# Kernel optimization log

Measured on AMD Instinct MI355X. Metric: run time of the kernel, lower is better.

Reference implementation:

```python
import jax, jax.numpy as jnp
import numpy as np

B, S, D = 4, 1024, 768
H = 12
DK = D // H            # 64
NUM_EMB = 10
MAX_DIST = 100000.0 * 2 ** 0.5
POS_SCALE = 100000.0   # tile positions live in [0, 100000]


def setup_inputs() -> dict:
    key = jax.random.key(0)
    ks = jax.random.split(key, 12)
    query = jax.random.normal(ks[0], (B, S, D), dtype=jnp.float32)
    key_t = jax.random.normal(ks[1], (B, S, D), dtype=jnp.float32)
    value = jax.random.normal(ks[2], (B, S, D), dtype=jnp.float32)
    tile_positions = jax.random.uniform(ks[3], (B, S, 2), dtype=jnp.float32) * POS_SCALE
    # Linear weights, torch layout [out, in]; xavier_uniform init, zero bias
    lim = float(np.sqrt(6.0 / (D + D)))
    Wq = jax.random.uniform(ks[4], (D, D), minval=-lim, maxval=lim, dtype=jnp.float32)
    Wk = jax.random.uniform(ks[5], (D, D), minval=-lim, maxval=lim, dtype=jnp.float32)
    Wv = jax.random.uniform(ks[6], (D, D), minval=-lim, maxval=lim, dtype=jnp.float32)
    bq = jnp.zeros((D,), jnp.float32)
    bk = jnp.zeros((D,), jnp.float32)
    bv = jnp.zeros((D,), jnp.float32)
    emb_k = jax.random.normal(ks[7], (NUM_EMB, DK), dtype=jnp.float32)  # nn.Embedding default N(0,1)
    return {"query": query, "key": key_t, "value": value,
            "tile_positions": tile_positions,
            "Wq": Wq, "bq": bq, "Wk": Wk, "bk": bk, "Wv": Wv, "bv": bv,
            "emb_k": emb_k}


def reference(query, key, value, tile_positions, Wq, bq, Wk, bk, Wv, bv, emb_k):
    b, s, _ = query.shape
    # projections -> [B, H, S, DK]
    q = (query @ Wq.T + bq).reshape(b, s, H, DK).transpose(0, 2, 1, 3)
    k = (key   @ Wk.T + bk).reshape(b, s, H, DK).transpose(0, 2, 1, 3)
    v = (value @ Wv.T + bv).reshape(b, s, H, DK).transpose(0, 2, 1, 3)
    # pairwise distances, normalized, discretized to embedding indices
    pos = jax.lax.stop_gradient(tile_positions)
    diff = pos[:, :, None, :] - pos[:, None, :, :]          # [B,S,S,2]
    dist = jnp.sqrt(jnp.sum(diff * diff, axis=-1)) / MAX_DIST  # [B,S,S]
    idx = jnp.clip(jnp.round(dist * (NUM_EMB - 1)), 0, NUM_EMB - 1).astype(jnp.int32)
    rk = emb_k[idx]                                          # [B,S,S,DK]
    # logits: QK^T plus distance-aware key bias
    attn_logits = jnp.einsum('bhqd,bhkd->bhqk', q, k)
    attn_logits = attn_logits + jnp.einsum('bhqd,bqkd->bhqk', q, rk)
    attn_logits = attn_logits / (DK ** 0.5)
    attention = jax.nn.softmax(attn_logits, axis=-1)
    out = jnp.einsum('bhqk,bhkd->bhqd', attention, v)       # [B,H,S,DK]
    out = out.transpose(0, 2, 1, 3).reshape(b, s, -1)       # [B,S,D]
    return out
```

## Files before the change

kernel.cpp:

```cpp
#include <hip/hip_runtime.h>
#include <hip/hip_bf16.h>

#define Bsz 4
#define Ssz 1024
#define Dsz 768
#define Hn 12
#define DKsz 64
#define NUMEMB 10

#define IDX_OFF 64
#define K_OFF   4194368
#define V_OFF   10485824
#define WBF_OFF 16777280
#define XBF_OFF 20316224
#define WS_TIER_B 20316224ULL
#define WS_TIER_A 39190592ULL

#define NXz 3145728
#define NWz 589824

typedef __attribute__((ext_vector_type(8))) short short8;
typedef __attribute__((ext_vector_type(8))) float float8;
typedef __attribute__((ext_vector_type(4))) float f32x4;
typedef __attribute__((ext_vector_type(4))) unsigned int u32x4;
typedef __attribute__((ext_vector_type(2))) unsigned int u32x2;
typedef __attribute__((ext_vector_type(4))) short s16x4;

__device__ __forceinline__ float bfbits2f(short u) {
    union { unsigned int i; float f; } v;
    v.i = ((unsigned int)(unsigned short)u) << 16;
    return v.f;
}
__device__ __forceinline__ unsigned short f2bf_bits(float f) {
    __hip_bfloat16 h = __float2bfloat16(f);
    return *reinterpret_cast<unsigned short*>(&h);
}

template<bool BF16>
__device__ __forceinline__ float loadf(const void* base, size_t idx) {
    if constexpr (BF16) return __bfloat162float(((const __hip_bfloat16*)base)[idx]);
    else return ((const float*)base)[idx];
}
template<bool BF16>
__device__ __forceinline__ short8 load8bf(const void* base, size_t idx) {
    if constexpr (BF16) {
        return *(const short8*)((const short*)base + idx);
    } else {
        float8 f = *(const float8*)((const float*)base + idx);
        short8 r;
#pragma unroll
        for (int i = 0; i < 8; i++) r[i] = (short)f2bf_bits(f[i]);
        return r;
    }
}
template<bool BF16>
__device__ __forceinline__ float8 load8f(const void* base, size_t idx) {
    if constexpr (BF16) {
        short8 s = *(const short8*)((const short*)base + idx);
        float8 f;
#pragma unroll
        for (int i = 0; i < 8; i++) f[i] = bfbits2f(s[i]);
        return f;
    } else {
        return *(const float8*)((const float*)base + idx);
    }
}

__global__ __launch_bounds__(64) void detect_kernel(
    const unsigned int* __restrict__ q, const unsigned int* __restrict__ p,
    const unsigned int* __restrict__ w, const unsigned int* __restrict__ e,
    int* __restrict__ flags)
{
    const int which = blockIdx.x;
    const unsigned int* ptr = (which == 0) ? q : ((which == 1) ? p : ((which == 2) ? w : e));
    const int n = (which == 3) ? 320 : ((which == 1) ? 4096 : 1024);
    int cnt = 0;
    for (int i = threadIdx.x; i < n; i += 64) {
        const unsigned int ex = (ptr[i] >> 7) & 0xFF;
        cnt += (ex >= 110 && ex <= 145) ? 1 : 0;
    }
#pragma unroll
    for (int off = 1; off < 64; off <<= 1) cnt += __shfl_xor(cnt, off, 64);
    if (threadIdx.x == 0) flags[which] = (2 * cnt > n) ? 1 : 0;
}

__global__ __launch_bounds__(256) void conv_kernel(
    const void* __restrict__ X0, const void* __restrict__ X1, const void* __restrict__ X2,
    const void* __restrict__ W0, const void* __restrict__ W1, const void* __restrict__ W2,
    const int* __restrict__ flags, short* __restrict__ Xbf, short* __restrict__ Wbf,
    int doX)
{
    const long t = (long)blockIdx.x * 256 + threadIdx.x;
    const bool xb = flags[0] != 0, wb = flags[2] != 0;
    if (doX) {
        const long i8 = t * 8;
        if (i8 < (long)3 * NXz) {
            const int z = (int)(i8 / NXz);
            const long off = i8 - (long)z * NXz;
            const void* X = (z == 0) ? X0 : ((z == 1) ? X1 : X2);
            short8 v = xb ? load8bf<true>(X, off) : load8bf<false>(X, off);
            *(short8*)(Xbf + i8) = v;
        } else {
            const long j = i8 - (long)3 * NXz;
            const int z = (int)(j / NWz);
            const long off = j - (long)z * NWz;
            const void* W = (z == 0) ? W0 : ((z == 1) ? W1 : W2);
            short8 v = wb ? load8bf<true>(W, off) : load8bf<false>(W, off);
            *(short8*)(Wbf + j) = v;
        }
    } else {
        const long j = t * 8;
        const int z = (int)(j / NWz);
        const long off = j - (long)z * NWz;
        const void* W = (z == 0) ? W0 : ((z == 1) ? W1 : W2);
        short8 v = wb ? load8bf<true>(W, off) : load8bf<false>(W, off);
        *(short8*)(Wbf + j) = v;
    }
}

template<bool PB>
__device__ __forceinline__ void idx_body(
    const void* pos, unsigned char* __restrict__ idxb)
{
    const int kt = blockIdx.x, qt = blockIdx.y, b = blockIdx.z;
    const int t = threadIdx.x;
    const int r = t >> 2, cc = t & 3;
    const int q = qt * 64 + r;
    const float qx = loadf<PB>(pos, ((size_t)b * Ssz + q) * 2);
    const float qy = loadf<PB>(pos, ((size_t)b * Ssz + q) * 2 + 1);
    const float MAXD = 141421.35623730951f;
    const int k0 = kt * 64 + cc * 16;
    unsigned int w[4];
#pragma unroll
    for (int g = 0; g < 4; g++) {
        unsigned int acc = 0;
#pragma unroll
        for (int u = 0; u < 4; u++) {
            const int k = k0 + g * 4 + u;
            const float kx = loadf<PB>(pos, ((size_t)b * Ssz + k) * 2);
            const float ky = loadf<PB>(pos, ((size_t)b * Ssz + k) * 2 + 1);
            const float dx = __fsub_rn(qx, kx);
            const float dy = __fsub_rn(qy, ky);
            const float ss = __fadd_rn(__fmul_rn(dx, dx), __fmul_rn(dy, dy));
            const float dist = __fdiv_rn(sqrtf(ss), MAXD);
            const float d9 = __fmul_rn(dist, 9.0f);
            int idx = (int)rintf(d9);
            idx = idx < 0 ? 0 : (idx > NUMEMB - 1 ? NUMEMB - 1 : idx);
            acc |= ((unsigned int)idx) << (8 * u);
        }
        w[g] = acc;
    }
    u32x4 v; v[0] = w[0]; v[1] = w[1]; v[2] = w[2]; v[3] = w[3];
    *(u32x4*)(idxb + ((size_t)(b * Ssz + q)) * Ssz + k0) = v;
}

__global__ __launch_bounds__(256) void idx_kernel(
    const void* pos, const int* __restrict__ flags, unsigned char* __restrict__ idxb)
{
    if (flags[1] != 0) idx_body<true >(pos, idxb);
    else               idx_body<false>(pos, idxb);
}

template<bool XB, bool WB>
__device__ __forceinline__ void proj_body(
    const void* X, const void* W, const void* bias, bool biasbf, void* Y, bool ybf,
    int zmode, int bx, int by, short* As, short* Bs)
{
    const int tid  = threadIdx.x;
    const int wave = tid >> 6;
    const int lane = tid & 63;
    const int l15  = lane & 15;
    const int quad = lane >> 4;
    const int wm = wave & 1;
    const int wn = wave >> 1;
    const int m0 = bx * 64;
    const int n0 = by * 128;

    f32x4 acc[2][4];
#pragma unroll
    for (int i = 0; i < 2; i++)
#pragma unroll
        for (int j = 0; j < 4; j++) acc[i][j] = (f32x4)0.0f;

    const int r0 = tid >> 3;
    const int cc = tid & 7;

    short8 pa0 = load8bf<XB>(X, (size_t)(m0 + r0)      * Dsz + cc * 8);
    short8 pa1 = load8bf<XB>(X, (size_t)(m0 + 32 + r0) * Dsz + cc * 8);
    short8 pb0 = load8bf<WB>(W, (size_t)(n0 + r0)      * Dsz + cc * 8);
    short8 pb1 = load8bf<WB>(W, (size_t)(n0 + 32 + r0) * Dsz + cc * 8);
    short8 pb2 = load8bf<WB>(W, (size_t)(n0 + 64 + r0) * Dsz + cc * 8);
    short8 pb3 = load8bf<WB>(W, (size_t)(n0 + 96 + r0) * Dsz + cc * 8);

    for (int kk = 0; kk < Dsz; kk += 64) {
        __syncthreads();
        *(short8*)&As[(r0)      * 72 + cc * 8] = pa0;
        *(short8*)&As[(32 + r0) * 72 + cc * 8] = pa1;
        *(short8*)&Bs[(r0)      * 72 + cc * 8] = pb0;
        *(short8*)&Bs[(32 + r0) * 72 + cc * 8] = pb1;
        *(short8*)&Bs[(64 + r0) * 72 + cc * 8] = pb2;
        *(short8*)&Bs[(96 + r0) * 72 + cc * 8] = pb3;
        __syncthreads();

        if (kk + 64 < Dsz) {
            const int k2 = kk + 64 + cc * 8;
            pa0 = load8bf<XB>(X, (size_t)(m0 + r0)      * Dsz + k2);
            pa1 = load8bf<XB>(X, (size_t)(m0 + 32 + r0) * Dsz + k2);
            pb0 = load8bf<WB>(W, (size_t)(n0 + r0)      * Dsz + k2);
            pb1 = load8bf<WB>(W, (size_t)(n0 + 32 + r0) * Dsz + k2);
            pb2 = load8bf<WB>(W, (size_t)(n0 + 64 + r0) * Dsz + k2);
            pb3 = load8bf<WB>(W, (size_t)(n0 + 96 + r0) * Dsz + k2);
        }

#pragma unroll
        for (int st = 0; st < 2; st++) {
            short8 af[2], bf[4];
#pragma unroll
            for (int i = 0; i < 2; i++)
                af[i] = *(const short8*)&As[(wm * 32 + i * 16 + l15) * 72 + st * 32 + quad * 8];
#pragma unroll
            for (int j = 0; j < 4; j++)
                bf[j] = *(const short8*)&Bs[(wn * 64 + j * 16 + l15) * 72 + st * 32 + quad * 8];
#pragma unroll
            for (int i = 0; i < 2; i++)
#pragma unroll
                for (int j = 0; j < 4; j++)
                    acc[i][j] = __builtin_amdgcn_mfma_f32_16x16x32_bf16(af[i], bf[j], acc[i][j], 0, 0, 0);
        }
    }

#pragma unroll
    for (int j = 0; j < 4; j++) {
        const int n = n0 + wn * 64 + j * 16 + l15;
        const float bv_ = biasbf ? loadf<true>(bias, n) : loadf<false>(bias, n);
        const int hh = n >> 6, dk = n & 63;
#pragma unroll
        for (int i = 0; i < 2; i++) {
            const int ms = m0 + wm * 32 + i * 16 + quad * 4;
            const int bb = ms >> 10;
            const int s0 = ms & 1023;
            if (zmode == 2) {
                s16x4 pkv;
#pragma unroll
                for (int r = 0; r < 4; r++) pkv[r] = (short)f2bf_bits(acc[i][j][r] + bv_);
                *(s16x4*)((short*)Y + (((size_t)bb * Hn + hh) * DKsz + dk) * Ssz + s0) = pkv;
            } else if (zmode == 1) {
#pragma unroll
                for (int r = 0; r < 4; r++)
                    ((__hip_bfloat16*)Y)[(((size_t)bb * Hn + hh) * Ssz + (s0 + r)) * DKsz + dk] =
                        __float2bfloat16(acc[i][j][r] + bv_);
            } else {
#pragma unroll
                for (int r = 0; r < 4; r++) {
                    const float val = acc[i][j][r] + bv_;
                    const size_t oi = (size_t)(ms + r) * Dsz + n;
                    if (ybf) ((__hip_bfloat16*)Y)[oi] = __float2bfloat16(val);
                    else     ((float*)Y)[oi] = val;
                }
            }
        }
    }
}

__global__ __launch_bounds__(256) void proj_kernel(
    const void* X0, const void* X1, const void* X2,
    const void* Wq, const void* bq, const void* Wk, const void* bk,
    const void* Wv, const void* bv,
    void* Qw, void* Kw, void* Vw, const int* __restrict__ flags,
    int fx, int fw)
{
    __shared__ __align__(16) short As[64 * 72];
    __shared__ __align__(16) short Bs[128 * 72];
    const int z = blockIdx.z;
    const void* X = (z == 0) ? X0 : ((z == 1) ? X1 : X2);
    const void* W = (z == 0) ? Wq : ((z == 1) ? Wk : Wv);
    const void* B = (z == 0) ? bq : ((z == 1) ? bk : bv);
    void* Y = (z == 0) ? Qw : ((z == 1) ? Kw : Vw);
    const bool xb = fx || flags[0] != 0;
    const bool wb = fw || flags[2] != 0;
    const bool biasbf = flags[2] != 0;
    const bool ybf = (flags[0] != 0) || (z != 0);
    if (xb) { if (wb) proj_body<true , true >(X, W, B, biasbf, Y, ybf, z, blockIdx.x, blockIdx.y, As, Bs);
              else    proj_body<true , false>(X, W, B, biasbf, Y, ybf, z, blockIdx.x, blockIdx.y, As, Bs); }
    else    { if (wb) proj_body<false, true >(X, W, B, biasbf, Y, ybf, z, blockIdx.x, blockIdx.y, As, Bs);
              else    proj_body<false, false>(X, W, B, biasbf, Y, ybf, z, blockIdx.x, blockIdx.y, As, Bs); }
}

template<bool QB, bool EB>
__device__ __forceinline__ void attn_body(
    const void* Qw, const short* __restrict__ Ks, const short* __restrict__ Vs,
    const unsigned char* __restrict__ idxb, const void* __restrict__ emb, void* out,
    unsigned short* Klds, unsigned short* Vtlds, float* qe)
{
    const int qt = blockIdx.x, h = blockIdx.y, b = blockIdx.z;
    const int tid  = threadIdx.x;
    const int wave = tid >> 6;
    const int lane = tid & 63;
    const int l15  = lane & 15;
    const int quad = lane >> 4;

    const float CSC = 0.18033688011112042f;

    for (int p = tid; p < 64 * NUMEMB; p += 256) {
        const int row = p / NUMEMB, e = p - row * NUMEMB;
        const size_t qoff = ((size_t)b * Ssz + qt * 64 + row) * Dsz + h * DKsz;
        float s = 0.f;
#pragma unroll
        for (int c = 0; c < 8; c++) {
            short8 qv = load8bf<QB>(Qw, qoff + c * 8);
            float8 ef = load8f<EB>(emb, (size_t)e * DKsz + c * 8);
#pragma unroll
            for (int i = 0; i < 8; i++) s += bfbits2f(qv[i]) * ef[i];
        }
        qe[p] = s * CSC;
    }

    short8 qfrag[2];
    {
        const size_t qbase = ((size_t)b * Ssz + qt * 64 + wave * 16 + l15) * Dsz + h * DKsz;
        qfrag[0] = load8bf<QB>(Qw, qbase + quad * 8);
        qfrag[1] = load8bf<QB>(Qw, qbase + 32 + quad * 8);
    }

    float m_run = -1e30f, l_run = 0.f;
    f32x4 oacc[4];
#pragma unroll
    for (int j = 0; j < 4; j++) oacc[j] = (f32x4)0.0f;

    const int r0 = tid >> 3, cc = tid & 7;
    const int ksl = (cc + 4 * (r0 & 1) - r0) & 7;
    const int kwoff = r0 * 72 + ksl * 8;
    const int vwoff = r0 * 72 + cc * 8;

    int koff[4][2];
#pragma unroll
    for (int jb = 0; jb < 4; jb++) {
        const int krow = (jb & 2) * 16 + (l15 >> 2) * 8 + (jb & 1) * 4 + (l15 & 3);
        const int base = quad + 4 * (l15 & 1) - (l15 & 3) + 8;
#pragma unroll
        for (int st = 0; st < 2; st++)
            koff[jb][st] = krow * 72 + ((base + 4 * (st ^ (jb & 1))) & 7) * 8;
    }

    const short* kp = Ks + ((size_t)(b * Hn + h) * Ssz) * DKsz + tid * 8;
    const short* vp = Vs + ((size_t)(b * Hn + h) * DKsz + r0) * Ssz + cc * 8;
    const unsigned char* ip = idxb + ((size_t)b * Ssz + qt * 64 + wave * 16 + l15) * Ssz + quad * 8;
    const int qrow10 = (wave * 16 + l15) * NUMEMB;

    short8 pk0 = *(const short8*)(kp);
    short8 pk1 = *(const short8*)(kp + 2048);
    short8 pv0 = *(const short8*)(vp);
    short8 pv1 = *(const short8*)(vp + 32 * Ssz);
    u32x2 idA = *(const u32x2*)(ip);
    u32x2 idB = *(const u32x2*)(ip + 32);

    *(short8*)&Klds[kwoff]            = pk0;
    *(short8*)&Klds[32 * 72 + kwoff]  = pk1;
    *(short8*)&Vtlds[vwoff]           = pv0;
    *(short8*)&Vtlds[32 * 72 + vwoff] = pv1;
    __syncthreads();

    for (int it = 0; it < 16; ++it) {
        const int cur = (it & 1) ? (64 * 72) : 0;
        const int nxt = (it & 1) ? 0 : (64 * 72);
        const unsigned int jd[4] = { idA[0], idA[1], idB[0], idB[1] };

        if (it + 1 < 16) {
            kp += 4096;
            vp += 64;
            ip += 64;
            pk0 = *(const short8*)(kp);
            pk1 = *(const short8*)(kp + 2048);
            pv0 = *(const short8*)(vp);
            pv1 = *(const short8*)(vp + 32 * Ssz);
            idA = *(const u32x2*)(ip);
            idB = *(const u32x2*)(ip + 32);
        }

        f32x4 sf[4];
#pragma unroll
        for (int jb = 0; jb < 4; jb++) sf[jb] = (f32x4)0.0f;
        __builtin_amdgcn_s_setprio(1);
#pragma unroll
        for (int st = 0; st < 2; st++) {
#pragma unroll
            for (int jb = 0; jb < 4; jb++) {
                short8 kf = *(const short8*)&Klds[cur + koff[jb][st]];
                sf[jb] = __builtin_amdgcn_mfma_f32_16x16x32_bf16(kf, qfrag[st], sf[jb], 0, 0, 0);
            }
        }
        __builtin_amdgcn_s_setprio(0);

        float sv[4][4];
#pragma unroll
        for (int jb = 0; jb < 4; jb++) {
            const unsigned int iw = jd[jb];
#pragma unroll
            for (int r = 0; r < 4; r++)
                sv[jb][r] = fmaf(sf[jb][r], CSC, qe[qrow10 + ((iw >> (8 * r)) & 0xFF)]);
        }

        float t0 = fmaxf(fmaxf(sv[0][0], sv[0][1]), fmaxf(sv[0][2], sv[0][3]));
        float t1 = fmaxf(fmaxf(sv[1][0], sv[1][1]), fmaxf(sv[1][2], sv[1][3]));
        float t2 = fmaxf(fmaxf(sv[2][0], sv[2][1]), fmaxf(sv[2][2], sv[2][3]));
        float t3 = fmaxf(fmaxf(sv[3][0], sv[3][1]), fmaxf(sv[3][2], sv[3][3]));
        float vmax = fmaxf(fmaxf(t0, t1), fmaxf(t2, t3));
        vmax = fmaxf(vmax, __shfl_xor(vmax, 16, 64));
        vmax = fmaxf(vmax, __shfl_xor(vmax, 32, 64));

        if (!__all(vmax - m_run <= 8.0f)) {
            const float mnew = fmaxf(m_run, vmax);
            const float alpha = exp2f(m_run - mnew);
            m_run = mnew;
            l_run *= alpha;
            float aO[4];
#pragma unroll
            for (int r = 0; r < 4; r++)
                aO[r] = __shfl(alpha, (lane & 48) | (quad * 4 + r), 64);
#pragma unroll
            for (int j = 0; j < 4; j++) {
                f32x4 o = oacc[j];
#pragma unroll
                for (int r = 0; r < 4; r++) o[r] *= aO[r];
                oacc[j] = o;
            }
        }

#pragma unroll
        for (int jb = 0; jb < 4; jb++)
#pragma unroll
            for (int r = 0; r < 4; r++)
                sv[jb][r] = exp2f(sv[jb][r] - m_run);

        float s0 = (sv[0][0] + sv[0][1]) + (sv[0][2] + sv[0][3]);
        float s1 = (sv[1][0] + sv[1][1]) + (sv[1][2] + sv[1][3]);
        float s2 = (sv[2][0] + sv[2][1]) + (sv[2][2] + sv[2][3]);
        float s3 = (sv[3][0] + sv[3][1]) + (sv[3][2] + sv[3][3]);
        float psum = (s0 + s1) + (s2 + s3);
        psum += __shfl_xor(psum, 16, 64);
        psum += __shfl_xor(psum, 32, 64);
        l_run += psum;

        short8 pa[2];
#pragma unroll
        for (int st = 0; st < 2; st++)
#pragma unroll
            for (int j = 0; j < 8; j++)
                pa[st][j] = (short)f2bf_bits(sv[2 * st + (j >> 2)][j & 3]);

        __builtin_amdgcn_s_setprio(1);
#pragma unroll
        for (int st = 0; st < 2; st++) {
#pragma unroll
            for (int j = 0; j < 4; j++) {
                short8 vb = *(const short8*)&Vtlds[cur + (j * 16 + l15) * 72 + st * 32 + quad * 8];
                oacc[j] = __builtin_amdgcn_mfma_f32_16x16x32_bf16(pa[st], vb, oacc[j], 0, 0, 0);
            }
        }
        __builtin_amdgcn_s_setprio(0);

        if (it + 1 < 16) {
            *(short8*)&Klds[nxt + kwoff]            = pk0;
            *(short8*)&Klds[nxt + 32 * 72 + kwoff]  = pk1;
            *(short8*)&Vtlds[nxt + vwoff]           = pv0;
            *(short8*)&Vtlds[nxt + 32 * 72 + vwoff] = pv1;
        }
        __syncthreads();
    }

    const float inv = 1.0f / l_run;
    float invO[4];
#pragma unroll
    for (int r = 0; r < 4; r++)
        invO[r] = __shfl(inv, (lane & 48) | (quad * 4 + r), 64);

#pragma unroll
    for (int r = 0; r < 4; r++) {
        const int m = qt * 64 + wave * 16 + quad * 4 + r;
#pragma unroll
        for (int j = 0; j < 4; j++) {
            const int n = h * DKsz + j * 16 + l15;
            const float val = oacc[j][r] * invO[r];
            const size_t oidx = ((size_t)b * Ssz + m) * Dsz + n;
            if constexpr (QB) ((__hip_bfloat16*)out)[oidx] = __float2bfloat16(val);
            else              ((float*)out)[oidx] = val;
        }
    }
}

__global__ __launch_bounds__(256) void attn_kernel(
    const void* Qw, const short* __restrict__ Ks, const short* __restrict__ Vs,
    const unsigned char* __restrict__ idxb, const void* __restrict__ emb, void* out,
    const int* __restrict__ flags)
{
    __shared__ __align__(16) unsigned short Klds[2 * 64 * 72];
    __shared__ __align__(16) unsigned short Vtlds[2 * 64 * 72];
    __shared__ __align__(16) float qe[64 * NUMEMB];

    const bool qb = flags[0] != 0, eb = flags[3] != 0;
    if (qb) { if (eb) attn_body<true , true >(Qw, Ks, Vs, idxb, emb, out, Klds, Vtlds, qe);
              else    attn_body<true , false>(Qw, Ks, Vs, idxb, emb, out, Klds, Vtlds, qe); }
    else    { if (eb) attn_body<false, true >(Qw, Ks, Vs, idxb, emb, out, Klds, Vtlds, qe);
              else    attn_body<false, false>(Qw, Ks, Vs, idxb, emb, out, Klds, Vtlds, qe); }
}

extern "C" void kernel_launch(void* const* d_in, const int* in_sizes, int n_in,
                              void* d_out, int out_size, void* d_ws, size_t ws_size,
                              hipStream_t stream) {
    const void* query = d_in[0];
    const void* key   = d_in[1];
    const void* value = d_in[2];
    const void* tpos  = d_in[3];
    const void* Wq    = d_in[4];
    const void* bq    = d_in[5];
    const void* Wk    = d_in[6];
    const void* bk    = d_in[7];
    const void* Wv    = d_in[8];
    const void* bv    = d_in[9];
    const void* emb   = d_in[10];

    int*           flags = (int*)d_ws;
    unsigned char* idxb  = (unsigned char*)d_ws + IDX_OFF;
    void*          Kw    = (char*)d_ws + K_OFF;
    void*          Vw    = (char*)d_ws + V_OFF;
    short*         Wbf   = (short*)((char*)d_ws + WBF_OFF);
    short*         Xbf   = (short*)((char*)d_ws + XBF_OFF);
    void*          Qw    = d_out;

    const bool tierA = ws_size >= WS_TIER_A;
    const bool tierB = !tierA && ws_size >= WS_TIER_B;

    detect_kernel<<<4, 64, 0, stream>>>(
        (const unsigned int*)query, (const unsigned int*)tpos,
        (const unsigned int*)Wq, (const unsigned int*)emb, flags);

    if (tierA)
        conv_kernel<<<5472, 256, 0, stream>>>(query, key, value, Wq, Wk, Wv, flags, Xbf, Wbf, 1);
    else if (tierB)
        conv_kernel<<<864, 256, 0, stream>>>(query, key, value, Wq, Wk, Wv, flags, Xbf, Wbf, 0);

    idx_kernel<<<dim3(16, 16, Bsz), 256, 0, stream>>>(tpos, flags, idxb);

    if (tierA)
        proj_kernel<<<dim3(64, 6, 3), 256, 0, stream>>>(
            Xbf, Xbf + NXz, Xbf + 2 * NXz,
            Wbf, bq, Wbf + NWz, bk, Wbf + 2 * NWz, bv,
            Qw, Kw, Vw, flags, 1, 1);
    else if (tierB)
        proj_kernel<<<dim3(64, 6, 3), 256, 0, stream>>>(
            query, key, value,
            Wbf, bq, Wbf + NWz, bk, Wbf + 2 * NWz, bv,
            Qw, Kw, Vw, flags, 0, 1);
    else
        proj_kernel<<<dim3(64, 6, 3), 256, 0, stream>>>(
            query, key, value, Wq, bq, Wk, bk, Wv, bv,
            Qw, Kw, Vw, flags, 0, 0);

    attn_kernel<<<dim3(16, Hn, Bsz), 256, 0, stream>>>(
        Qw, (const short*)Kw, (const short*)Vw, idxb, emb, d_out, flags);
}
```

Before: 207.5 us.

## Add double-buffered direct-to-LDS projection GEMM and replicate qe table per quad

Adds a projection kernel for the bf16-workspace tier that loads tiles straight from global memory into LDS with global_load_lds. It double-buffers the tiles and uses an XOR swizzle, so the next K-tile loads while MFMAs run on the current one and register staging is avoided. Separately, the attention kernel's per-row distance-bias table in LDS is replicated four times with padded strides, one copy per lane quad, to cut bank conflicts on the indexed lookups. The trade-off is more LDS use and a wait on all outstanding loads at every iteration, which may limit how much load and compute overlap.

```diff
diff --git a/kernel.cpp b/kernel.cpp
--- a/kernel.cpp
+++ b/kernel.cpp
@@ -19,6 +19,9 @@
 #define NXz 3145728
 #define NWz 589824
 
+#define QE_RS 12
+#define QE_QS 776
+
 typedef __attribute__((ext_vector_type(8))) short short8;
 typedef __attribute__((ext_vector_type(8))) float float8;
 typedef __attribute__((ext_vector_type(4))) float f32x4;
@@ -34,6 +37,12 @@
 __device__ __forceinline__ unsigned short f2bf_bits(float f) {
     __hip_bfloat16 h = __float2bfloat16(f);
     return *reinterpret_cast<unsigned short*>(&h);
+}
+
+__device__ __forceinline__ void gld16(const short* g, short* l) {
+    __builtin_amdgcn_global_load_lds(
+        (const __attribute__((address_space(1))) void*)g,
+        (__attribute__((address_space(3))) void*)l, 16, 0, 0);
 }
 
 template<bool BF16>
@@ -161,6 +170,43 @@
     else               idx_body<false>(pos, idxb);
 }
 
+__device__ __forceinline__ void proj_epilogue(
+    f32x4 (&acc)[2][4], const void* bias, bool biasbf, void* Y, bool ybf,
+    int zmode, int m0, int n0, int wm, int wn, int l15, int quad)
+{
+#pragma unroll
+    for (int j = 0; j < 4; j++) {
+        const int n = n0 + wn * 64 + j * 16 + l15;
+        const float bv_ = biasbf ? loadf<true>(bias, n) : loadf<false>(bias, n);
+        const int hh = n >> 6, dk = n & 63;
+#pragma unroll
+        for (int i = 0; i < 2; i++) {
+            const int ms = m0 + wm * 32 + i * 16 + quad * 4;
+            const int bb = ms >> 10;
+            const int s0 = ms & 1023;
+            if (zmode == 2) {
+                s16x4 pkv;
+#pragma unroll
+                for (int r = 0; r < 4; r++) pkv[r] = (short)f2bf_bits(acc[i][j][r] + bv_);
+                *(s16x4*)((short*)Y + (((size_t)bb * Hn + hh) * DKsz + dk) * Ssz + s0) = pkv;
+            } else if (zmode == 1) {
+#pragma unroll
+                for (int r = 0; r < 4; r++)
+                    ((__hip_bfloat16*)Y)[(((size_t)bb * Hn + hh) * Ssz + (s0 + r)) * DKsz + dk] =
+                        __float2bfloat16(acc[i][j][r] + bv_);
+            } else {
+#pragma unroll
+                for (int r = 0; r < 4; r++) {
+                    const float val = acc[i][j][r] + bv_;
+                    const size_t oi = (size_t)(ms + r) * Dsz + n;
+                    if (ybf) ((__hip_bfloat16*)Y)[oi] = __float2bfloat16(val);
+                    else     ((float*)Y)[oi] = val;
+                }
+            }
+        }
+    }
+}
+
 template<bool XB, bool WB>
 __device__ __forceinline__ void proj_body(
     const void* X, const void* W, const void* bias, bool biasbf, void* Y, bool ybf,
@@ -228,38 +274,7 @@
                     acc[i][j] = __builtin_amdgcn_mfma_f32_16x16x32_bf16(af[i], bf[j], acc[i][j], 0, 0, 0);
         }
     }
-
-#pragma unroll
-    for (int j = 0; j < 4; j++) {
-        const int n = n0 + wn * 64 + j * 16 + l15;
-        const float bv_ = biasbf ? loadf<true>(bias, n) : loadf<false>(bias, n);
-        const int hh = n >> 6, dk = n & 63;
-#pragma unroll
-        for (int i = 0; i < 2; i++) {
-            const int ms = m0 + wm * 32 + i * 16 + quad * 4;
-            const int bb = ms >> 10;
-            const int s0 = ms & 1023;
-            if (zmode == 2) {
-                s16x4 pkv;
-#pragma unroll
-                for (int r = 0; r < 4; r++) pkv[r] = (short)f2bf_bits(acc[i][j][r] + bv_);
-                *(s16x4*)((short*)Y + (((size_t)bb * Hn + hh) * DKsz + dk) * Ssz + s0) = pkv;
-            } else if (zmode == 1) {
-#pragma unroll
-                for (int r = 0; r < 4; r++)
-                    ((__hip_bfloat16*)Y)[(((size_t)bb * Hn + hh) * Ssz + (s0 + r)) * DKsz + dk] =
-                        __float2bfloat16(acc[i][j][r] + bv_);
-            } else {
-#pragma unroll
-                for (int r = 0; r < 4; r++) {
-                    const float val = acc[i][j][r] + bv_;
-                    const size_t oi = (size_t)(ms + r) * Dsz + n;
-                    if (ybf) ((__hip_bfloat16*)Y)[oi] = __float2bfloat16(val);
-                    else     ((float*)Y)[oi] = val;
-                }
-            }
-        }
-    }
+    proj_epilogue(acc, bias, biasbf, Y, ybf, zmode, m0, n0, wm, wn, l15, quad);
 }
 
 __global__ __launch_bounds__(256) void proj_kernel(
@@ -286,6 +301,87 @@
               else    proj_body<false, false>(X, W, B, biasbf, Y, ybf, z, blockIdx.x, blockIdx.y, As, Bs); }
 }
 
+__global__ __launch_bounds__(256) void proj_lds_kernel(
+    const short* __restrict__ Xbf, const short* __restrict__ Wbf,
+    const void* bq, const void* bk, const void* bv,
+    void* Qw, void* Kw, void* Vw, const int* __restrict__ flags)
+{
+    __shared__ __align__(16) short As[2][64 * 64];
+    __shared__ __align__(16) short Bs[2][128 * 64];
+
+    const int z = blockIdx.z;
+    const short* X = Xbf + (size_t)z * NXz;
+    const short* W = Wbf + (size_t)z * NWz;
+    const void* Bp = (z == 0) ? bq : ((z == 1) ? bk : bv);
+    void* Y = (z == 0) ? Qw : ((z == 1) ? Kw : Vw);
+    const bool biasbf = flags[2] != 0;
+    const bool ybf = (flags[0] != 0) || (z != 0);
+
+    const int tid  = threadIdx.x;
+    const int wave = tid >> 6;
+    const int lane = tid & 63;
+    const int l15  = lane & 15;
+    const int quad = lane >> 4;
+    const int wm = wave & 1;
+    const int wn = wave >> 1;
+    const int m0 = blockIdx.x * 64;
+    const int n0 = blockIdx.y * 128;
+
+    f32x4 acc[2][4];
+#pragma unroll
+    for (int i = 0; i < 2; i++)
+#pragma unroll
+        for (int j = 0; j < 4; j++) acc[i][j] = (f32x4)0.0f;
+
+    const int sr = lane >> 3;
+    const int sc = lane & 7;
+    const int gch = (sc ^ sr) * 8;
+
+    const short* ga = X + (size_t)(m0 + wave * 16 + sr) * Dsz + gch;
+    const short* gb = W + (size_t)(n0 + wave * 32 + sr) * Dsz + gch;
+
+    auto STAGE = [&](int bb, int kk) {
+        const short* gA = ga + kk;
+        gld16(gA,            &As[bb][(wave * 16     ) * 64]);
+        gld16(gA + 8 * Dsz,  &As[bb][(wave * 16 + 8 ) * 64]);
+        const short* gB = gb + kk;
+        gld16(gB,            &Bs[bb][(wave * 32     ) * 64]);
+        gld16(gB + 8 * Dsz,  &Bs[bb][(wave * 32 + 8 ) * 64]);
+        gld16(gB + 16 * Dsz, &Bs[bb][(wave * 32 + 16) * 64]);
+        gld16(gB + 24 * Dsz, &Bs[bb][(wave * 32 + 24) * 64]);
+    };
+
+    STAGE(0, 0);
+    asm volatile("s_waitcnt vmcnt(0)" ::: "memory");
+    __builtin_amdgcn_s_barrier();
+
+    for (int t = 0; t < 12; ++t) {
+        const int cb = t & 1;
+        if (t + 1 < 12) STAGE(cb ^ 1, (t + 1) * 64);
+
+#pragma unroll
+        for (int st = 0; st < 2; st++) {
+            const int slot = ((st * 4 + quad) ^ (l15 & 7)) * 8;
+            short8 af[2], bf[4];
+#pragma unroll
+            for (int i = 0; i < 2; i++)
+                af[i] = *(const short8*)&As[cb][(wm * 32 + i * 16 + l15) * 64 + slot];
+#pragma unroll
+            for (int j = 0; j < 4; j++)
+                bf[j] = *(const short8*)&Bs[cb][(wn * 64 + j * 16 + l15) * 64 + slot];
+#pragma unroll
+            for (int i = 0; i < 2; i++)
+#pragma unroll
+                for (int j = 0; j < 4; j++)
+                    acc[i][j] = __builtin_amdgcn_mfma_f32_16x16x32_bf16(af[i], bf[j], acc[i][j], 0, 0, 0);
+        }
+
+        asm volatile("s_waitcnt vmcnt(0)" ::: "memory");
+        __builtin_amdgcn_s_barrier();
+    }
+    proj_epilogue(acc, Bp, biasbf, Y, ybf, z, m0, n0, wm, wn, l15, quad);
+}
+
 template<bool QB, bool EB>
 __device__ __forceinline__ void attn_body(
     const void* Qw, const short* __restrict__ Ks, const short* __restrict__ Vs,
@@ -312,7 +408,9 @@
 #pragma unroll
             for (int i = 0; i < 8; i++) s += bfbits2f(qv[i]) * ef[i];
         }
-        qe[p] = s * CSC;
+        const float val = s * CSC;
+#pragma unroll
+        for (int qd = 0; qd < 4; qd++) qe[qd * QE_QS + row * QE_RS + e] = val;
     }
 
     short8 qfrag[2];
@@ -345,7 +443,7 @@
     const short* kp = Ks + ((size_t)(b * Hn + h) * Ssz) * DKsz + tid * 8;
     const short* vp = Vs + ((size_t)(b * Hn + h) * DKsz + r0) * Ssz + cc * 8;
     const unsigned char* ip = idxb + ((size_t)b * Ssz + qt * 64 + wave * 16 + l15) * Ssz + quad * 8;
-    const int qrow10 = (wave * 16 + l15) * NUMEMB;
+    const float* qeL = qe + quad * QE_QS + (wave * 16 + l15) * QE_RS;
 
     short8 pk0 = *(const short8*)(kp);
     short8 pk1 = *(const short8*)(kp + 2048);
@@ -397,7 +495,7 @@
             const unsigned int iw = jd[jb];
 #pragma unroll
             for (int r = 0; r < 4; r++)
-                sv[jb][r] = fmaf(sf[jb][r], CSC, qe[qrow10 + ((iw >> (8 * r)) & 0xFF)]);
+                sv[jb][r] = fmaf(sf[jb][r], CSC, qeL[(iw >> (8 * r)) & 0xFF]);
         }
 
         float t0 = fmaxf(fmaxf(sv[0][0], sv[0][1]), fmaxf(sv[0][2], sv[0][3]));
@@ -495,7 +593,7 @@
 {
     __shared__ __align__(16) unsigned short Klds[2 * 64 * 72];
     __shared__ __align__(16) unsigned short Vtlds[2 * 64 * 72];
-    __shared__ __align__(16) float qe[64 * NUMEMB];
+    __shared__ __align__(16) float qe[4 * QE_QS];
 
     const bool qb = flags[0] != 0, eb = flags[3] != 0;
     if (qb) { if (eb) attn_body<true , true >(Qw, Ks, Vs, idxb, emb, out, Klds, Vtlds, qe);
@@ -542,10 +640,8 @@
     idx_kernel<<<dim3(16, 16, Bsz), 256, 0, stream>>>(tpos, flags, idxb);
 
     if (tierA)
-        proj_kernel<<<dim3(64, 6, 3), 256, 0, stream>>>(
-            Xbf, Xbf + NXz, Xbf + 2 * NXz,
-            Wbf, bq, Wbf + NWz, bk, Wbf + 2 * NWz, bv,
-            Qw, Kw, Vw, flags, 1, 1);
+        proj_lds_kernel<<<dim3(64, 6, 3), 256, 0, stream>>>(
+            Xbf, Wbf, bq, bk, bv, Qw, Kw, Vw, flags);
     else if (tierB)
         proj_kernel<<<dim3(64, 6, 3), 256, 0, stream>>>(
             query, key, value,
```

Result: slower. 211.8 us (+2.1%).

## Software-pipeline QK^T one tile ahead, XOR-swizzle LDS, fold dtype detection into conv

Applied to the files above, without the earlier changes.

The attention loop now computes the next tile's QK^T MFMAs before running softmax and PV on the current tile, with a two-deep register prefetch of K, V and the distance indices, and it splits the K and V LDS writes around the barrier. LDS tiles drop the padded 72-element stride for a 64-element stride with XOR swizzling, and the qe table is replicated per quad to reduce LDS bank conflicts on the embedding-bias lookup. The separate dtype-detect launch is removed on the conv tiers: every conv block recomputes the vote itself, and blocks 0, 1 and 3 write the flags. This saves one launch but adds redundant global reads in every conv block, and it relies on the flag writes finishing before later kernels on the same stream.

```diff
diff --git a/kernel.cpp b/kernel.cpp
--- a/kernel.cpp
+++ b/kernel.cpp
@@ -19,6 +19,9 @@
 #define NXz 3145728
 #define NWz 589824
 
+#define KVHALF 4096
+#define QE_RS 40
+
 typedef __attribute__((ext_vector_type(8))) short short8;
 typedef __attribute__((ext_vector_type(8))) float float8;
 typedef __attribute__((ext_vector_type(4))) float f32x4;
@@ -34,6 +37,17 @@
 __device__ __forceinline__ unsigned short f2bf_bits(float f) {
     __hip_bfloat16 h = __float2bfloat16(f);
     return *reinterpret_cast<unsigned short*>(&h);
+}
+
+__device__ __forceinline__ int dtvote(const unsigned int* p, int n) {
+    int cnt = 0;
+    for (int i = (threadIdx.x & 63); i < n; i += 64) {
+        const unsigned int ex = (p[i] >> 7) & 0xFF;
+        cnt += (ex >= 110 && ex <= 145) ? 1 : 0;
+    }
+#pragma unroll
+    for (int off = 1; off < 64; off <<= 1) cnt += __shfl_xor(cnt, off, 64);
+    return (2 * cnt > n) ? 1 : 0;
 }
 
 template<bool BF16>
@@ -74,24 +88,29 @@
     const int which = blockIdx.x;
     const unsigned int* ptr = (which == 0) ? q : ((which == 1) ? p : ((which == 2) ? w : e));
     const int n = (which == 3) ? 320 : ((which == 1) ? 4096 : 1024);
-    int cnt = 0;
-    for (int i = threadIdx.x; i < n; i += 64) {
-        const unsigned int ex = (ptr[i] >> 7) & 0xFF;
-        cnt += (ex >= 110 && ex <= 145) ? 1 : 0;
-    }
-#pragma unroll
-    for (int off = 1; off < 64; off <<= 1) cnt += __shfl_xor(cnt, off, 64);
-    if (threadIdx.x == 0) flags[which] = (2 * cnt > n) ? 1 : 0;
+    const int f = dtvote(ptr, n);
+    if (threadIdx.x == 0) flags[which] = f;
 }
 
 __global__ __launch_bounds__(256) void conv_kernel(
     const void* __restrict__ X0, const void* __restrict__ X1, const void* __restrict__ X2,
     const void* __restrict__ W0, const void* __restrict__ W1, const void* __restrict__ W2,
-    const int* __restrict__ flags, short* __restrict__ Xbf, short* __restrict__ Wbf,
+    const void* __restrict__ tpos, const void* __restrict__ emb,
+    int* __restrict__ flags, short* __restrict__ Xbf, short* __restrict__ Wbf,
     int doX)
 {
+    if (blockIdx.x == 1) {
+        const int f = dtvote((const unsigned int*)tpos, 1024);
+        if (threadIdx.x == 0) flags[1] = f;
+    } else if (blockIdx.x == 3) {
+        const int f = dtvote((const unsigned int*)emb, 320);
+        if (threadIdx.x == 0) flags[3] = f;
+    }
+    const bool xb = dtvote((const unsigned int*)X0, 256) != 0;
+    const bool wb = dtvote((const unsigned int*)W0, 256) != 0;
+    if (blockIdx.x == 0 && threadIdx.x == 0) { flags[0] = xb ? 1 : 0; flags[2] = wb ? 1 : 0; }
+
     const long t = (long)blockIdx.x * 256 + threadIdx.x;
-    const bool xb = flags[0] != 0, wb = flags[2] != 0;
     if (doX) {
         const long i8 = t * 8;
         if (i8 < (long)3 * NXz) {
@@ -312,7 +331,9 @@
 #pragma unroll
             for (int i = 0; i < 8; i++) s += bfbits2f(qv[i]) * ef[i];
         }
-        qe[p] = s * CSC;
+        const float val = s * CSC;
+#pragma unroll
+        for (int q = 0; q < 4; q++) qe[row * QE_RS + q * 10 + e] = val;
     }
 
     short8 qfrag[2];
@@ -328,76 +349,96 @@
     for (int j = 0; j < 4; j++) oacc[j] = (f32x4)0.0f;
 
     const int r0 = tid >> 3, cc = tid & 7;
-    const int ksl = (cc + 4 * (r0 & 1) - r0) & 7;
-    const int kwoff = r0 * 72 + ksl * 8;
-    const int vwoff = r0 * 72 + cc * 8;
-
+    const int swr   = (r0 & 3) | (((r0 >> 3) & 1) << 2);
+    const int wroff = r0 * 64 + (cc ^ swr) * 8;
+
+    const int swk = (l15 & 3) | (((l15 >> 2) & 1) << 2);
+    const int vsw = (l15 & 3) | (((l15 >> 3) & 1) << 2);
     int koff[4][2];
 #pragma unroll
     for (int jb = 0; jb < 4; jb++) {
         const int krow = (jb & 2) * 16 + (l15 >> 2) * 8 + (jb & 1) * 4 + (l15 & 3);
-        const int base = quad + 4 * (l15 & 1) - (l15 & 3) + 8;
 #pragma unroll
         for (int st = 0; st < 2; st++)
-            koff[jb][st] = krow * 72 + ((base + 4 * (st ^ (jb & 1))) & 7) * 8;
-    }
+            koff[jb][st] = krow * 64 + ((st * 4 + quad) ^ swk) * 8;
+    }
+    int voff[2];
+#pragma unroll
+    for (int st = 0; st < 2; st++) voff[st] = ((st * 4 + quad) ^ vsw) * 8;
 
     const short* kp = Ks + ((size_t)(b * Hn + h) * Ssz) * DKsz + tid * 8;
     const short* vp = Vs + ((size_t)(b * Hn + h) * DKsz + r0) * Ssz + cc * 8;
     const unsigned char* ip = idxb + ((size_t)b * Ssz + qt * 64 + wave * 16 + l15) * Ssz + quad * 8;
-    const int qrow10 = (wave * 16 + l15) * NUMEMB;
+    const float* qeL = qe + (wave * 16 + l15) * QE_RS + quad * 10;
 
     short8 pk0 = *(const short8*)(kp);
     short8 pk1 = *(const short8*)(kp + 2048);
     short8 pv0 = *(const short8*)(vp);
     short8 pv1 = *(const short8*)(vp + 32 * Ssz);
-    u32x2 idA = *(const u32x2*)(ip);
-    u32x2 idB = *(const u32x2*)(ip + 32);
-
-    *(short8*)&Klds[kwoff]            = pk0;
-    *(short8*)&Klds[32 * 72 + kwoff]  = pk1;
-    *(short8*)&Vtlds[vwoff]           = pv0;
-    *(short8*)&Vtlds[32 * 72 + vwoff] = pv1;
+    u32x2 ic0 = *(const u32x2*)(ip);
+    u32x2 ic1 = *(const u32x2*)(ip + 32);
+
+    *(short8*)&Klds[wroff]            = pk0;
+    *(short8*)&Klds[32 * 64 + wroff]  = pk1;
+    *(short8*)&Vtlds[wroff]           = pv0;
+    *(short8*)&Vtlds[32 * 64 + wroff] = pv1;
+
+    kp += 4096; vp += 64; ip += 64;
+    pk0 = *(const short8*)(kp);
+    pk1 = *(const short8*)(kp + 2048);
+    pv0 = *(const short8*)(vp);
+    pv1 = *(const short8*)(vp + 32 * Ssz);
+    u32x2 in0 = *(const u32x2*)(ip);
+    u32x2 in1 = *(const u32x2*)(ip + 32);
+
     __syncthreads();
 
+    f32x4 sfc[4];
+#pragma unroll
+    for (int jb = 0; jb < 4; jb++) sfc[jb] = (f32x4)0.0f;
+    __builtin_amdgcn_s_setprio(1);
+#pragma unroll
+    for (int st = 0; st < 2; st++)
+#pragma unroll
+        for (int jb = 0; jb < 4; jb++) {
+            short8 kf = *(const short8*)&Klds[koff[jb][st]];
+            sfc[jb] = __builtin_amdgcn_mfma_f32_16x16x32_bf16(kf, qfrag[st], sfc[jb], 0, 0, 0);
+        }
+    __builtin_amdgcn_s_setprio(0);
+
     for (int it = 0; it < 16; ++it) {
-        const int cur = (it & 1) ? (64 * 72) : 0;
-        const int nxt = (it & 1) ? 0 : (64 * 72);
-        const unsigned int jd[4] = { idA[0], idA[1], idB[0], idB[1] };
+        const int bufn = ((it + 1) & 1) * KVHALF;
+        const int bufc = (it & 1) * KVHALF;
 
         if (it + 1 < 16) {
-            kp += 4096;
-            vp += 64;
-            ip += 64;
-            pk0 = *(const short8*)(kp);
-            pk1 = *(const short8*)(kp + 2048);
-            pv0 = *(const short8*)(vp);
-            pv1 = *(const short8*)(vp + 32 * Ssz);
-            idA = *(const u32x2*)(ip);
-            idB = *(const u32x2*)(ip + 32);
-        }
-
-        f32x4 sf[4];
-#pragma unroll
-        for (int jb = 0; jb < 4; jb++) sf[jb] = (f32x4)0.0f;
-        __builtin_amdgcn_s_setprio(1);
-#pragma unroll
-        for (int st = 0; st < 2; st++) {
-#pragma unroll
-            for (int jb = 0; jb < 4; jb++) {
-                short8 kf = *(const short8*)&Klds[cur + koff[jb][st]];
-                sf[jb] = __builtin_amdgcn_mfma_f32_16x16x32_bf16(kf, qfrag[st], sf[jb], 0, 0, 0);
-            }
-        }
-        __builtin_amdgcn_s_setprio(0);
-
+            *(short8*)&Klds[bufn + wroff]           = pk0;
+            *(short8*)&Klds[bufn + 32 * 64 + wroff] = pk1;
+        }
+        __syncthreads();
+
+        f32x4 sfn[4];
+#pragma unroll
+        for (int jb = 0; jb < 4; jb++) sfn[jb] = (f32x4)0.0f;
+        if (it + 1 < 16) {
+            __builtin_amdgcn_s_setprio(1);
+#pragma unroll
+            for (int st = 0; st < 2; st++)
+#pragma unroll
+                for (int jb = 0; jb < 4; jb++) {
+                    short8 kf = *(const short8*)&Klds[bufn + koff[jb][st]];
+                    sfn[jb] = __builtin_amdgcn_mfma_f32_16x16x32_bf16(kf, qfrag[st], sfn[jb], 0, 0, 0);
+                }
+            __builtin_amdgcn_s_setprio(0);
+        }
+
+        const unsigned int jd[4] = { ic0[0], ic0[1], ic1[0], ic1[1] };
         float sv[4][4];
 #pragma unroll
         for (int jb = 0; jb < 4; jb++) {
             const unsigned int iw = jd[jb];
 #pragma unroll
             for (int r = 0; r < 4; r++)
-                sv[jb][r] = fmaf(sf[jb][r], CSC, qe[qrow10 + ((iw >> (8 * r)) & 0xFF)]);
+                sv[jb][r] = fmaf(sfc[jb][r], CSC, qeL[(iw >> (8 * r)) & 0xFF]);
         }
 
         float t0 = fmaxf(fmaxf(sv[0][0], sv[0][1]), fmaxf(sv[0][2], sv[0][3]));
@@ -453,19 +494,32 @@
         for (int st = 0; st < 2; st++) {
 #pragma unroll
             for (int j = 0; j < 4; j++) {
-                short8 vb = *(const short8*)&Vtlds[cur + (j * 16 + l15) * 72 + st * 32 + quad * 8];
+                short8 vb = *(const short8*)&Vtlds[bufc + (j * 16 + l15) * 64 + voff[st]];
                 oacc[j] = __builtin_amdgcn_mfma_f32_16x16x32_bf16(pa[st], vb, oacc[j], 0, 0, 0);
             }
         }
         __builtin_amdgcn_s_setprio(0);
 
         if (it + 1 < 16) {
-            *(short8*)&Klds[nxt + kwoff]            = pk0;
-            *(short8*)&Klds[nxt + 32 * 72 + kwoff]  = pk1;
-            *(short8*)&Vtlds[nxt + vwoff]           = pv0;
-            *(short8*)&Vtlds[nxt + 32 * 72 + vwoff] = pv1;
-        }
-        __syncthreads();
+            *(short8*)&Vtlds[bufn + wroff]           = pv0;
+            *(short8*)&Vtlds[bufn + 32 * 64 + wroff] = pv1;
+        }
+
+        u32x2 lf0 = in0, lf1 = in1;
+        if (it + 2 < 16) {
+            kp += 4096; vp += 64; ip += 64;
+            pk0 = *(const short8*)(kp);
+            pk1 = *(const short8*)(kp + 2048);
+            pv0 = *(const short8*)(vp);
+            pv1 = *(const short8*)(vp + 32 * Ssz);
+            lf0 = *(const u32x2*)(ip);
+            lf1 = *(const u32x2*)(ip + 32);
+        }
+
+#pragma unroll
+        for (int jb = 0; jb < 4; jb++) sfc[jb] = sfn[jb];
+        ic0 = in0; ic1 = in1;
+        in0 = lf0; in1 = lf1;
     }
 
     const float inv = 1.0f / l_run;
@@ -493,9 +547,9 @@
     const unsigned char* __restrict__ idxb, const void* __restrict__ emb, void* out,
     const int* __restrict__ flags)
 {
-    __shared__ __align__(16) unsigned short Klds[2 * 64 * 72];
-    __shared__ __align__(16) unsigned short Vtlds[2 * 64 * 72];
-    __shared__ __align__(16) float qe[64 * NUMEMB];
+    __shared__ __align__(16) unsigned short Klds[2 * KVHALF];
+    __shared__ __align__(16) unsigned short Vtlds[2 * KVHALF];
+    __shared__ __align__(16) float qe[64 * QE_RS];
 
     const bool qb = flags[0] != 0, eb = flags[3] != 0;
     if (qb) { if (eb) attn_body<true , true >(Qw, Ks, Vs, idxb, emb, out, Klds, Vtlds, qe);
@@ -530,31 +584,31 @@
     const bool tierA = ws_size >= WS_TIER_A;
     const bool tierB = !tierA && ws_size >= WS_TIER_B;
 
-    detect_kernel<<<4, 64, 0, stream>>>(
-        (const unsigned int*)query, (const unsigned int*)tpos,
-        (const unsigned int*)Wq, (const unsigned int*)emb, flags);
-
-    if (tierA)
-        conv_kernel<<<5472, 256, 0, stream>>>(query, key, value, Wq, Wk, Wv, flags, Xbf, Wbf, 1);
-    else if (tierB)
-        conv_kernel<<<864, 256, 0, stream>>>(query, key, value, Wq, Wk, Wv, flags, Xbf, Wbf, 0);
-
-    idx_kernel<<<dim3(16, 16, Bsz), 256, 0, stream>>>(tpos, flags, idxb);
-
-    if (tierA)
+    if (tierA) {
+        conv_kernel<<<5472, 256, 0, stream>>>(query, key, value, Wq, Wk, Wv,
+                                              tpos, emb, flags, Xbf, Wbf, 1);
+        idx_kernel<<<dim3(16, 16, Bsz), 256, 0, stream>>>(tpos, flags, idxb);
         proj_kernel<<<dim3(64, 6, 3), 256, 0, stream>>>(
             Xbf, Xbf + NXz, Xbf + 2 * NXz,
             Wbf, bq, Wbf + NWz, bk, Wbf + 2 * NWz, bv,
             Qw, Kw, Vw, flags, 1, 1);
-    else if (tierB)
+    } else if (tierB) {
+        conv_kernel<<<864, 256, 0, stream>>>(query, key, value, Wq, Wk, Wv,
+                                             tpos, emb, flags, Xbf, Wbf, 0);
+        idx_kernel<<<dim3(16, 16, Bsz), 256, 0, stream>>>(tpos, flags, idxb);
         proj_kernel<<<dim3(64, 6, 3), 256, 0, stream>>>(
             query, key, value,
             Wbf, bq, Wbf + NWz, bk, Wbf + 2 * NWz, bv,
             Qw, Kw, Vw, flags, 0, 1);
-    else
+    } else {
+        detect_kernel<<<4, 64, 0, stream>>>(
+            (const unsigned int*)query, (const unsigned int*)tpos,
+            (const unsigned int*)Wq, (const unsigned int*)emb, flags);
+        idx_kernel<<<dim3(16, 16, Bsz), 256, 0, stream>>>(tpos, flags, idxb);
         proj_kernel<<<dim3(64, 6, 3), 256, 0, stream>>>(
             query, key, value, Wq, bq, Wk, bk, Wv, bv,
             Qw, Kw, Vw, flags, 0, 0);
+    }
 
     attn_kernel<<<dim3(16, Hn, Bsz), 256, 0, stream>>>(
         Qw, (const short*)Kw, (const short*)Vw, idxb, emb, d_out, flags);
```

New measurement: 224.1 us. 8.0% more time.

## Triple-buffer K/V in LDS with XOR swizzle and software-pipelined QK^T

Applied to the files above, without the earlier changes.

Replaces the padded double-buffered K/V LDS tiles with unpadded, XOR-swizzled triple buffers, and prefetches global K/V/index data two tiles ahead. The QK^T MFMAs for the next tile are issued before the softmax and PV of the current tile, so matrix work overlaps the scalar softmax phase. The aim is to hide global and LDS latency and avoid bank conflicts without padding, at the cost of more registers (a second score accumulator and extra index prefetch registers) and a more complex buffer rotation that can hurt occupancy.

```diff
diff --git a/kernel.cpp b/kernel.cpp
--- a/kernel.cpp
+++ b/kernel.cpp
@@ -18,6 +18,8 @@
 
 #define NXz 3145728
 #define NWz 589824
+
+#define KVBUF 4096
 
 typedef __attribute__((ext_vector_type(8))) short short8;
 typedef __attribute__((ext_vector_type(8))) float float8;
@@ -328,19 +330,22 @@
     for (int j = 0; j < 4; j++) oacc[j] = (f32x4)0.0f;
 
     const int r0 = tid >> 3, cc = tid & 7;
-    const int ksl = (cc + 4 * (r0 & 1) - r0) & 7;
-    const int kwoff = r0 * 72 + ksl * 8;
-    const int vwoff = r0 * 72 + cc * 8;
-
+    const int swr   = (r0 & 3) | (((r0 >> 3) & 1) << 2);
+    const int wroff = r0 * 64 + (cc ^ swr) * 8;
+
+    const int swk = (l15 & 3) | (((l15 >> 2) & 1) << 2);
+    const int vsw = (l15 & 3) | (((l15 >> 3) & 1) << 2);
     int koff[4][2];
 #pragma unroll
     for (int jb = 0; jb < 4; jb++) {
         const int krow = (jb & 2) * 16 + (l15 >> 2) * 8 + (jb & 1) * 4 + (l15 & 3);
-        const int base = quad + 4 * (l15 & 1) - (l15 & 3) + 8;
 #pragma unroll
         for (int st = 0; st < 2; st++)
-            koff[jb][st] = krow * 72 + ((base + 4 * (st ^ (jb & 1))) & 7) * 8;
-    }
+            koff[jb][st] = krow * 64 + ((st * 4 + quad) ^ swk) * 8;
+    }
+    int voff[2];
+#pragma unroll
+    for (int st = 0; st < 2; st++) voff[st] = ((st * 4 + quad) ^ vsw) * 8;
 
     const short* kp = Ks + ((size_t)(b * Hn + h) * Ssz) * DKsz + tid * 8;
     const short* vp = Vs + ((size_t)(b * Hn + h) * DKsz + r0) * Ssz + cc * 8;
@@ -351,53 +356,95 @@
     short8 pk1 = *(const short8*)(kp + 2048);
     short8 pv0 = *(const short8*)(vp);
     short8 pv1 = *(const short8*)(vp + 32 * Ssz);
-    u32x2 idA = *(const u32x2*)(ip);
-    u32x2 idB = *(const u32x2*)(ip + 32);
-
-    *(short8*)&Klds[kwoff]            = pk0;
-    *(short8*)&Klds[32 * 72 + kwoff]  = pk1;
-    *(short8*)&Vtlds[vwoff]           = pv0;
-    *(short8*)&Vtlds[32 * 72 + vwoff] = pv1;
+    u32x2 jcA = *(const u32x2*)(ip);
+    u32x2 jcB = *(const u32x2*)(ip + 32);
+    *(short8*)&Klds[wroff]            = pk0;
+    *(short8*)&Klds[32 * 64 + wroff]  = pk1;
+    *(short8*)&Vtlds[wroff]           = pv0;
+    *(short8*)&Vtlds[32 * 64 + wroff] = pv1;
+
+    kp += 4096; vp += 64; ip += 64;
+    pk0 = *(const short8*)(kp);
+    pk1 = *(const short8*)(kp + 2048);
+    pv0 = *(const short8*)(vp);
+    pv1 = *(const short8*)(vp + 32 * Ssz);
+    u32x2 j1A = *(const u32x2*)(ip);
+    u32x2 j1B = *(const u32x2*)(ip + 32);
+    *(short8*)&Klds[KVBUF + wroff]            = pk0;
+    *(short8*)&Klds[KVBUF + 32 * 64 + wroff]  = pk1;
+    *(short8*)&Vtlds[KVBUF + wroff]           = pv0;
+    *(short8*)&Vtlds[KVBUF + 32 * 64 + wroff] = pv1;
+
+    kp += 4096; vp += 64; ip += 64;
+    pk0 = *(const short8*)(kp);
+    pk1 = *(const short8*)(kp + 2048);
+    pv0 = *(const short8*)(vp);
+    pv1 = *(const short8*)(vp + 32 * Ssz);
+    u32x2 j2A = *(const u32x2*)(ip);
+    u32x2 j2B = *(const u32x2*)(ip + 32);
+
     __syncthreads();
 
+    f32x4 sfc[4];
+#pragma unroll
+    for (int jb = 0; jb < 4; jb++) sfc[jb] = (f32x4)0.0f;
+    __builtin_amdgcn_s_setprio(1);
+#pragma unroll
+    for (int st = 0; st < 2; st++)
+#pragma unroll
+        for (int jb = 0; jb < 4; jb++) {
+            short8 kf = *(const short8*)&Klds[koff[jb][st]];
+            sfc[jb] = __builtin_amdgcn_mfma_f32_16x16x32_bf16(kf, qfrag[st], sfc[jb], 0, 0, 0);
+        }
+    __builtin_amdgcn_s_setprio(0);
+
+    int bP = 0, bA = KVBUF, bW = 2 * KVBUF;
+
     for (int it = 0; it < 16; ++it) {
-        const int cur = (it & 1) ? (64 * 72) : 0;
-        const int nxt = (it & 1) ? 0 : (64 * 72);
-        const unsigned int jd[4] = { idA[0], idA[1], idB[0], idB[1] };
-
-        if (it + 1 < 16) {
-            kp += 4096;
-            vp += 64;
-            ip += 64;
+        const unsigned int jd0 = jcA[0], jd1 = jcA[1], jd2 = jcB[0], jd3 = jcB[1];
+
+        if (it + 2 < 16) {
+            *(short8*)&Klds[bW + wroff]            = pk0;
+            *(short8*)&Klds[bW + 32 * 64 + wroff]  = pk1;
+            *(short8*)&Vtlds[bW + wroff]           = pv0;
+            *(short8*)&Vtlds[bW + 32 * 64 + wroff] = pv1;
+        }
+        jcA = j1A; jcB = j1B; j1A = j2A; j1B = j2B;
+        if (it + 3 < 16) {
+            kp += 4096; vp += 64; ip += 64;
             pk0 = *(const short8*)(kp);
             pk1 = *(const short8*)(kp + 2048);
             pv0 = *(const short8*)(vp);
             pv1 = *(const short8*)(vp + 32 * Ssz);
-            idA = *(const u32x2*)(ip);
-            idB = *(const u32x2*)(ip + 32);
-        }
-
-        f32x4 sf[4];
-#pragma unroll
-        for (int jb = 0; jb < 4; jb++) sf[jb] = (f32x4)0.0f;
-        __builtin_amdgcn_s_setprio(1);
-#pragma unroll
-        for (int st = 0; st < 2; st++) {
+            j2A = *(const u32x2*)(ip);
+            j2B = *(const u32x2*)(ip + 32);
+        }
+
+        f32x4 sfn[4];
+#pragma unroll
+        for (int jb = 0; jb < 4; jb++) sfn[jb] = (f32x4)0.0f;
+        if (it + 1 < 16) {
+            __builtin_amdgcn_s_setprio(1);
+#pragma unroll
+            for (int st = 0; st < 2; st++)
+#pragma unroll
+                for (int jb = 0; jb < 4; jb++) {
+                    short8 kf = *(const short8*)&Klds[bA + koff[jb][st]];
+                    sfn[jb] = __builtin_amdgcn_mfma_f32_16x16x32_bf16(kf, qfrag[st], sfn[jb], 0, 0, 0);
+                }
+            __builtin_amdgcn_s_setprio(0);
+        }
+
+        float sv[4][4];
+        {
+            const unsigned int jw[4] = { jd0, jd1, jd2, jd3 };
 #pragma unroll
             for (int jb = 0; jb < 4; jb++) {
-                short8 kf = *(const short8*)&Klds[cur + koff[jb][st]];
-                sf[jb] = __builtin_amdgcn_mfma_f32_16x16x32_bf16(kf, qfrag[st], sf[jb], 0, 0, 0);
+                const unsigned int iw = jw[jb];
+#pragma unroll
+                for (int r = 0; r < 4; r++)
+                    sv[jb][r] = fmaf(sfc[jb][r], CSC, qe[qrow10 + ((iw >> (8 * r)) & 0xFF)]);
             }
-        }
-        __builtin_amdgcn_s_setprio(0);
-
-        float sv[4][4];
-#pragma unroll
-        for (int jb = 0; jb < 4; jb++) {
-            const unsigned int iw = jd[jb];
-#pragma unroll
-            for (int r = 0; r < 4; r++)
-                sv[jb][r] = fmaf(sf[jb][r], CSC, qe[qrow10 + ((iw >> (8 * r)) & 0xFF)]);
         }
 
         float t0 = fmaxf(fmaxf(sv[0][0], sv[0][1]), fmaxf(sv[0][2], sv[0][3]));
@@ -453,19 +500,17 @@
         for (int st = 0; st < 2; st++) {
 #pragma unroll
             for (int j = 0; j < 4; j++) {
-                short8 vb = *(const short8*)&Vtlds[cur + (j * 16 + l15) * 72 + st * 32 + quad * 8];
+                short8 vb = *(const short8*)&Vtlds[bP + (j * 16 + l15) * 64 + voff[st]];
                 oacc[j] = __builtin_amdgcn_mfma_f32_16x16x32_bf16(pa[st], vb, oacc[j], 0, 0, 0);
             }
         }
         __builtin_amdgcn_s_setprio(0);
 
-        if (it + 1 < 16) {
-            *(short8*)&Klds[nxt + kwoff]            = pk0;
-            *(short8*)&Klds[nxt + 32 * 72 + kwoff]  = pk1;
-            *(short8*)&Vtlds[nxt + vwoff]           = pv0;
-            *(short8*)&Vtlds[nxt + 32 * 72 + vwoff] = pv1;
-        }
         __syncthreads();
+
+#pragma unroll
+        for (int jb = 0; jb < 4; jb++) sfc[jb] = sfn[jb];
+        const int tmp = bP; bP = bA; bA = bW; bW = tmp;
     }
 
     const float inv = 1.0f / l_run;
@@ -493,8 +538,8 @@
     const unsigned char* __restrict__ idxb, const void* __restrict__ emb, void* out,
     const int* __restrict__ flags)
 {
-    __shared__ __align__(16) unsigned short Klds[2 * 64 * 72];
-    __shared__ __align__(16) unsigned short Vtlds[2 * 64 * 72];
+    __shared__ __align__(16) unsigned short Klds[3 * KVBUF];
+    __shared__ __align__(16) unsigned short Vtlds[3 * KVBUF];
     __shared__ __align__(16) float qe[64 * NUMEMB];
 
     const bool qb = flags[0] != 0, eb = flags[3] != 0;
```

New measurement: 213.5 us. 1.03x slower.
